# Kernel tuning notes

Measured on AMD Instinct MI355X. Metric: run time of the kernel, lower is better.

## Reference

```python
import jax, jax.numpy as jnp
import numpy as np

B, T, D_IN = 4096, 1024, 2
EMD, CELL, D_OUT = 128, 128, 5


def setup_inputs() -> dict:
    key = jax.random.key(0)
    ks = jax.random.split(key, 9)
    s = lambda k, shape, fan: jax.random.normal(k, shape, jnp.float32) / np.sqrt(fan)
    return {
        "inputs": jax.random.normal(ks[0], (B, T, D_IN), jnp.float32),
        "We": s(ks[1], (EMD, D_IN), D_IN),
        "be": s(ks[2], (EMD,), D_IN),
        "W_ih": s(ks[3], (4 * CELL, EMD), EMD),
        "W_hh": s(ks[4], (4 * CELL, CELL), CELL),
        "b_ih": s(ks[5], (4 * CELL,), CELL),
        "b_hh": s(ks[6], (4 * CELL,), CELL),
        "Wo": s(ks[7], (D_OUT, CELL), CELL),
        "bo": s(ks[8], (D_OUT,), CELL),
    }


def reference(inputs, We, be, W_ih, W_hh, b_ih, b_hh, Wo, bo):
    """VanillaLSTM forward: per-step embed MLP -> LSTMCell -> output MLP.
    inputs: [B, T, D_IN]; returns (outputs [B, T, D_OUT], h [B,CELL], c [B,CELL])."""
    Bsz = inputs.shape[0]
    cell = W_hh.shape[1]

    def step(hc, x_t):
        h, c = hc
        # input embedding MLP (Linear + ReLU, batch_norm=False)
        e = jax.nn.relu(x_t @ We.T + be)                      # [B, EMD]
        # torch.nn.LSTMCell gate math
        gates = e @ W_ih.T + b_ih + h @ W_hh.T + b_hh         # [B, 4*CELL]
        i, f, g, o = jnp.split(gates, 4, axis=-1)
        i, f, o = jax.nn.sigmoid(i), jax.nn.sigmoid(f), jax.nn.sigmoid(o)
        g = jnp.tanh(g)
        c_new = f * c + i * g
        h_new = o * jnp.tanh(c_new)
        # output embedding (Linear, no activation)
        y = h_new @ Wo.T + bo                                 # [B, D_OUT]
        return (h_new, c_new), y

    h0 = jnp.zeros((Bsz, cell), inputs.dtype)
    c0 = jnp.zeros((Bsz, cell), inputs.dtype)
    xs = jnp.swapaxes(inputs, 0, 1)                           # [T, B, D_IN]
    (h, c), ys = jax.lax.scan(step, (h0, c0), xs)
    outputs = jnp.swapaxes(ys, 0, 1)                          # [B, T, D_OUT]
    return outputs, h, c
```

## Files before the change

### kernel.cpp

```cpp
#include <hip/hip_runtime.h>
#include <hip/hip_bf16.h>


#define B_TOT 4096
#define T_LEN 1024
#define D_INP 2
#define EMD   128
#define CELL  128
#define D_OUT 5

#define ROWS  16
#define WAVES 8
#define BLOCK (WAVES * 64)
#define LDH   136

typedef short s8v  __attribute__((ext_vector_type(8)));
typedef short s4v  __attribute__((ext_vector_type(4)));
typedef float f32x4 __attribute__((ext_vector_type(4)));

#if __has_builtin(__builtin_amdgcn_exp2f)
#define EXP2F(x) __builtin_amdgcn_exp2f(x)
#else
#define EXP2F(x) exp2f(x)
#endif
#if __has_builtin(__builtin_amdgcn_rcpf)
#define RCPF(x) __builtin_amdgcn_rcpf(x)
#else
#define RCPF(x) (1.0f / (x))
#endif

__device__ __forceinline__ float bf2f(short s) {
    unsigned int u = ((unsigned int)(unsigned short)s) << 16;
    return __builtin_bit_cast(float, u);
}
__device__ __forceinline__ short f2bf(float f) {
    unsigned int u = __builtin_bit_cast(unsigned int, f);
    u += 0x7fffu + ((u >> 16) & 1u);
    return (short)(u >> 16);
}
__device__ __forceinline__ float sigm(float x) {
    return RCPF(1.0f + EXP2F(-1.44269504f * x));
}
__device__ __forceinline__ float tanh_fast(float x) {
    return 2.0f * RCPF(1.0f + EXP2F(-2.88539008f * x)) - 1.0f;
}
__device__ __forceinline__ s8v load8_f32_to_bf16(const float* p) {
    float4 a = *(const float4*)p;
    float4 b = *(const float4*)(p + 4);
    s8v r;
    r[0] = f2bf(a.x); r[1] = f2bf(a.y); r[2] = f2bf(a.z); r[3] = f2bf(a.w);
    r[4] = f2bf(b.x); r[5] = f2bf(b.y); r[6] = f2bf(b.z); r[7] = f2bf(b.w);
    return r;
}

__global__ __launch_bounds__(BLOCK, 1)
void lstm_persistent(const float* __restrict__ x,
                     const float* __restrict__ We,
                     const float* __restrict__ be,
                     const float* __restrict__ Wih,
                     const float* __restrict__ Whh,
                     const float* __restrict__ bih,
                     const float* __restrict__ bhh,
                     const float* __restrict__ Wo,
                     const float* __restrict__ bo,
                     float* __restrict__ out)
{
    __shared__ short h_lds[2][ROWS][LDH];
    __shared__ short e_lds[2][ROWS][LDH];

    const int tid  = threadIdx.x;
    const int lane = tid & 63;
    const int w    = tid >> 6;
    const int n16  = lane & 15;
    const int q    = lane >> 4;
    const int q8   = q * 8;
    const int b0   = blockIdx.x * ROWS;
    const int jcol = w * 16 + n16;

    float* out_y = out;
    float* out_h = out + (size_t)B_TOT * T_LEN * D_OUT;
    float* out_c = out_h + (size_t)B_TOT * CELL;

    s8v wih_f[4][4], whh_f[4][4];
    #pragma unroll
    for (int g = 0; g < 4; ++g) {
        const int row = g * CELL + jcol;
        #pragma unroll
        for (int kt = 0; kt < 4; ++kt) {
            wih_f[g][kt] = load8_f32_to_bf16(Wih + row * EMD  + kt * 32 + q8);
            whh_f[g][kt] = load8_f32_to_bf16(Whh + row * CELL + kt * 32 + q8);
        }
    }
    float bias_g[4];
    #pragma unroll
    for (int g = 0; g < 4; ++g)
        bias_g[g] = bih[g * CELL + jcol] + bhh[g * CELL + jcol];

    s8v wo_f[4];
    float bo_v = 0.0f;
    {
        s8v z = {0, 0, 0, 0, 0, 0, 0, 0};
        #pragma unroll
        for (int kt = 0; kt < 4; ++kt) wo_f[kt] = z;
        if (w == 0 && n16 < D_OUT) {
            #pragma unroll
            for (int kt = 0; kt < 4; ++kt)
                wo_f[kt] = load8_f32_to_bf16(Wo + n16 * CELL + kt * 32 + q8);
            bo_v = bo[n16];
        }
    }

    const int er  = tid >> 5;
    const int jj0 = (tid & 31) * 4;
    float weA[4], weB[4], bev[4];
    #pragma unroll
    for (int jl = 0; jl < 4; ++jl) {
        weA[jl] = We[(jj0 + jl) * 2 + 0];
        weB[jl] = We[(jj0 + jl) * 2 + 1];
        bev[jl] = be[jj0 + jl];
    }
    const float* xrow = x + (size_t)(b0 + er) * T_LEN * D_INP;

    {
        unsigned int* hz = (unsigned int*)&h_lds[0][0][0];
        for (int i = tid; i < ROWS * LDH / 2; i += BLOCK) hz[i] = 0u;

        float2 xd = *(const float2*)(xrow);
        s4v ev;
        #pragma unroll
        for (int jl = 0; jl < 4; ++jl)
            ev[jl] = f2bf(fmaxf(xd.x * weA[jl] + xd.y * weB[jl] + bev[jl], 0.0f));
        *(s4v*)&e_lds[0][er][jj0] = ev;
    }

    float c_r[4] = {0.0f, 0.0f, 0.0f, 0.0f};

    #pragma unroll 1
    for (int u = 0; u < T_LEN; ++u) {
        const int p = u & 1;
        __syncthreads();

        s8v ah[4], ae[4];
        #pragma unroll
        for (int kt = 0; kt < 4; ++kt) {
            ah[kt] = *(const s8v*)&h_lds[p][n16][kt * 32 + q8];
            ae[kt] = *(const s8v*)&e_lds[p][n16][kt * 32 + q8];
        }

        if (w == 0 && u > 0) {
            f32x4 ay = {bo_v, bo_v, bo_v, bo_v};
            #pragma unroll
            for (int kt = 0; kt < 4; ++kt)
                ay = __builtin_amdgcn_mfma_f32_16x16x32_bf16(ah[kt], wo_f[kt], ay, 0, 0, 0);
            if (n16 < D_OUT) {
                #pragma unroll
                for (int r = 0; r < 4; ++r)
                    out_y[((size_t)(b0 + q * 4 + r) * T_LEN + (u - 1)) * D_OUT + n16] = ay[r];
            }
        }

        f32x4 acc[4];
        #pragma unroll
        for (int g = 0; g < 4; ++g) {
            f32x4 a = {bias_g[g], bias_g[g], bias_g[g], bias_g[g]};
            #pragma unroll
            for (int kt = 0; kt < 4; ++kt) {
                a = __builtin_amdgcn_mfma_f32_16x16x32_bf16(ah[kt], whh_f[g][kt], a, 0, 0, 0);
                a = __builtin_amdgcn_mfma_f32_16x16x32_bf16(ae[kt], wih_f[g][kt], a, 0, 0, 0);
            }
            acc[g] = a;
        }

        #pragma unroll
        for (int r = 0; r < 4; ++r) {
            float iv = sigm(acc[0][r]);
            float fv = sigm(acc[1][r]);
            float gv = tanh_fast(acc[2][r]);
            float ov = sigm(acc[3][r]);
            c_r[r] = fv * c_r[r] + iv * gv;
            float hv = ov * tanh_fast(c_r[r]);
            h_lds[1 - p][q * 4 + r][jcol] = f2bf(hv);
        }

        {
            const int tn = (u + 1 < T_LEN) ? (u + 1) : (T_LEN - 1);
            float2 xd = *(const float2*)(xrow + tn * D_INP);
            s4v ev;
            #pragma unroll
            for (int jl = 0; jl < 4; ++jl)
                ev[jl] = f2bf(fmaxf(xd.x * weA[jl] + xd.y * weB[jl] + bev[jl], 0.0f));
            *(s4v*)&e_lds[1 - p][er][jj0] = ev;
        }
    }

    __syncthreads();

    if (w == 0) {
        s8v ah[4];
        #pragma unroll
        for (int kt = 0; kt < 4; ++kt)
            ah[kt] = *(const s8v*)&h_lds[0][n16][kt * 32 + q8];
        f32x4 ay = {bo_v, bo_v, bo_v, bo_v};
        #pragma unroll
        for (int kt = 0; kt < 4; ++kt)
            ay = __builtin_amdgcn_mfma_f32_16x16x32_bf16(ah[kt], wo_f[kt], ay, 0, 0, 0);
        if (n16 < D_OUT) {
            #pragma unroll
            for (int r = 0; r < 4; ++r)
                out_y[((size_t)(b0 + q * 4 + r) * T_LEN + (T_LEN - 1)) * D_OUT + n16] = ay[r];
        }
    }

    #pragma unroll
    for (int r = 0; r < 4; ++r)
        out_c[(size_t)(b0 + q * 4 + r) * CELL + jcol] = c_r[r];

    {
        const int m  = (tid * 4) >> 7;
        const int k0 = (tid * 4) & 127;
        s4v hv = *(const s4v*)&h_lds[0][m][k0];
        float4 hf;
        hf.x = bf2f(hv[0]); hf.y = bf2f(hv[1]);
        hf.z = bf2f(hv[2]); hf.w = bf2f(hv[3]);
        *(float4*)(out_h + (size_t)(b0 + m) * CELL + k0) = hf;
    }
}

extern "C" void kernel_launch(void* const* d_in, const int* in_sizes, int n_in,
                              void* d_out, int out_size, void* d_ws, size_t ws_size,
                              hipStream_t stream) {
    const float* x   = (const float*)d_in[0];
    const float* We  = (const float*)d_in[1];
    const float* be  = (const float*)d_in[2];
    const float* Wih = (const float*)d_in[3];
    const float* Whh = (const float*)d_in[4];
    const float* bih = (const float*)d_in[5];
    const float* bhh = (const float*)d_in[6];
    const float* Wo  = (const float*)d_in[7];
    const float* bo  = (const float*)d_in[8];
    float* out = (float*)d_out;

    dim3 grid(B_TOT / ROWS);
    dim3 block(BLOCK);
    hipLaunchKernelGGL(lstm_persistent, grid, block, 0, stream,
                       x, We, be, Wih, Whh, bih, bhh, Wo, bo, out);
}
```

Measured before the change: 1.398 ms.

## Transpose MFMA operands so each lane owns four channels and packs stores

Swaps the A/B operands of every MFMA so the accumulator holds four consecutive cell channels per lane for one batch row. This lets the h state be written to LDS as two packed 32-bit bf16 words instead of four scattered shorts, and lets the output y, c and final h be stored as contiguous vectors. It also replaces __syncthreads with a raw s_waitcnt lgkmcnt+s_barrier and hoists the next x load ahead of the MFMA work to hide global latency. The bf16 packing now rounds half-up instead of round-to-nearest-even, and the final h is written in fp32 rather than round-tripped through bf16.

Result: no change. 1.394 ms (-0.3%).

```diff
diff --git a/kernel.cpp b/kernel.cpp
--- a/kernel.cpp
+++ b/kernel.cpp
@@ -17,6 +17,8 @@
 typedef short s8v  __attribute__((ext_vector_type(8)));
 typedef short s4v  __attribute__((ext_vector_type(4)));
 typedef float f32x4 __attribute__((ext_vector_type(4)));
+
+#define BAR() asm volatile("s_waitcnt lgkmcnt(0)\n\ts_barrier" ::: "memory")
 
 #if __has_builtin(__builtin_amdgcn_exp2f)
 #define EXP2F(x) __builtin_amdgcn_exp2f(x)
@@ -37,6 +39,11 @@
     unsigned int u = __builtin_bit_cast(unsigned int, f);
     u += 0x7fffu + ((u >> 16) & 1u);
     return (short)(u >> 16);
+}
+__device__ __forceinline__ unsigned int pk_bf16(float a, float b) {
+    unsigned int ua = __builtin_bit_cast(unsigned int, a);
+    unsigned int ub = __builtin_bit_cast(unsigned int, b);
+    return ((ua + 0x8000u) >> 16) | ((ub + 0x8000u) & 0xffff0000u);
 }
 __device__ __forceinline__ float sigm(float x) {
     return RCPF(1.0f + EXP2F(-1.44269504f * x));
@@ -75,7 +82,7 @@
     const int q    = lane >> 4;
     const int q8   = q * 8;
     const int b0   = blockIdx.x * ROWS;
-    const int jcol = w * 16 + n16;
+    const int ch0  = w * 16 + q * 4;
 
     float* out_y = out;
     float* out_h = out + (size_t)B_TOT * T_LEN * D_OUT;
@@ -84,20 +91,23 @@
     s8v wih_f[4][4], whh_f[4][4];
     #pragma unroll
     for (int g = 0; g < 4; ++g) {
-        const int row = g * CELL + jcol;
+        const int row = g * CELL + w * 16 + n16;
         #pragma unroll
         for (int kt = 0; kt < 4; ++kt) {
             wih_f[g][kt] = load8_f32_to_bf16(Wih + row * EMD  + kt * 32 + q8);
             whh_f[g][kt] = load8_f32_to_bf16(Whh + row * CELL + kt * 32 + q8);
         }
     }
-    float bias_g[4];
+    float4 bias4[4];
     #pragma unroll
-    for (int g = 0; g < 4; ++g)
-        bias_g[g] = bih[g * CELL + jcol] + bhh[g * CELL + jcol];
+    for (int g = 0; g < 4; ++g) {
+        float4 bi = *(const float4*)(bih + g * CELL + ch0);
+        float4 bh = *(const float4*)(bhh + g * CELL + ch0);
+        bias4[g] = make_float4(bi.x + bh.x, bi.y + bh.y, bi.z + bh.z, bi.w + bh.w);
+    }
 
     s8v wo_f[4];
-    float bo_v = 0.0f;
+    float bo_r[4];
     {
         s8v z = {0, 0, 0, 0, 0, 0, 0, 0};
         #pragma unroll
@@ -106,7 +116,11 @@
             #pragma unroll
             for (int kt = 0; kt < 4; ++kt)
                 wo_f[kt] = load8_f32_to_bf16(Wo + n16 * CELL + kt * 32 + q8);
-            bo_v = bo[n16];
+        }
+        #pragma unroll
+        for (int r = 0; r < 4; ++r) {
+            const int oc = q * 4 + r;
+            bo_r[r] = (w == 0 && oc < D_OUT) ? bo[oc] : 0.0f;
         }
     }
 
@@ -126,11 +140,13 @@
         for (int i = tid; i < ROWS * LDH / 2; i += BLOCK) hz[i] = 0u;
 
         float2 xd = *(const float2*)(xrow);
-        s4v ev;
-        #pragma unroll
-        for (int jl = 0; jl < 4; ++jl)
-            ev[jl] = f2bf(fmaxf(xd.x * weA[jl] + xd.y * weB[jl] + bev[jl], 0.0f));
-        *(s4v*)&e_lds[0][er][jj0] = ev;
+        float e0 = fmaxf(xd.x * weA[0] + xd.y * weB[0] + bev[0], 0.0f);
+        float e1 = fmaxf(xd.x * weA[1] + xd.y * weB[1] + bev[1], 0.0f);
+        float e2 = fmaxf(xd.x * weA[2] + xd.y * weB[2] + bev[2], 0.0f);
+        float e3 = fmaxf(xd.x * weA[3] + xd.y * weB[3] + bev[3], 0.0f);
+        unsigned int u01 = pk_bf16(e0, e1), u23 = pk_bf16(e2, e3);
+        *(unsigned int*)&e_lds[0][er][jj0]     = u01;
+        *(unsigned int*)&e_lds[0][er][jj0 + 2] = u23;
     }
 
     float c_r[4] = {0.0f, 0.0f, 0.0f, 0.0f};
@@ -138,7 +154,10 @@
     #pragma unroll 1
     for (int u = 0; u < T_LEN; ++u) {
         const int p = u & 1;
-        __syncthreads();
+        BAR();
+
+        const int tn = (u + 1 < T_LEN) ? (u + 1) : (T_LEN - 1);
+        float2 xd = *(const float2*)(xrow + tn * D_INP);
 
         s8v ah[4], ae[4];
         #pragma unroll
@@ -148,29 +167,31 @@
         }
 
         if (w == 0 && u > 0) {
-            f32x4 ay = {bo_v, bo_v, bo_v, bo_v};
+            f32x4 ay = {bo_r[0], bo_r[1], bo_r[2], bo_r[3]};
             #pragma unroll
             for (int kt = 0; kt < 4; ++kt)
-                ay = __builtin_amdgcn_mfma_f32_16x16x32_bf16(ah[kt], wo_f[kt], ay, 0, 0, 0);
-            if (n16 < D_OUT) {
-                #pragma unroll
-                for (int r = 0; r < 4; ++r)
-                    out_y[((size_t)(b0 + q * 4 + r) * T_LEN + (u - 1)) * D_OUT + n16] = ay[r];
+                ay = __builtin_amdgcn_mfma_f32_16x16x32_bf16(wo_f[kt], ah[kt], ay, 0, 0, 0);
+            float* yp = out_y + ((size_t)(b0 + n16) * T_LEN + (u - 1)) * D_OUT;
+            if (q == 0) {
+                yp[0] = ay[0]; yp[1] = ay[1]; yp[2] = ay[2]; yp[3] = ay[3];
+            } else if (q == 1) {
+                yp[4] = ay[0];
             }
         }
 
         f32x4 acc[4];
         #pragma unroll
         for (int g = 0; g < 4; ++g) {
-            f32x4 a = {bias_g[g], bias_g[g], bias_g[g], bias_g[g]};
+            f32x4 a = {bias4[g].x, bias4[g].y, bias4[g].z, bias4[g].w};
             #pragma unroll
             for (int kt = 0; kt < 4; ++kt) {
-                a = __builtin_amdgcn_mfma_f32_16x16x32_bf16(ah[kt], whh_f[g][kt], a, 0, 0, 0);
-                a = __builtin_amdgcn_mfma_f32_16x16x32_bf16(ae[kt], wih_f[g][kt], a, 0, 0, 0);
+                a = __builtin_amdgcn_mfma_f32_16x16x32_bf16(whh_f[g][kt], ah[kt], a, 0, 0, 0);
+                a = __builtin_amdgcn_mfma_f32_16x16x32_bf16(wih_f[g][kt], ae[kt], a, 0, 0, 0);
             }
             acc[g] = a;
         }
 
+        float hv[4];
         #pragma unroll
         for (int r = 0; r < 4; ++r) {
             float iv = sigm(acc[0][r]);
@@ -178,52 +199,51 @@
             float gv = tanh_fast(acc[2][r]);
             float ov = sigm(acc[3][r]);
             c_r[r] = fv * c_r[r] + iv * gv;
-            float hv = ov * tanh_fast(c_r[r]);
-            h_lds[1 - p][q * 4 + r][jcol] = f2bf(hv);
-        }
-
+            hv[r] = ov * tanh_fast(c_r[r]);
+        }
         {
-            const int tn = (u + 1 < T_LEN) ? (u + 1) : (T_LEN - 1);
-            float2 xd = *(const float2*)(xrow + tn * D_INP);
-            s4v ev;
-            #pragma unroll
-            for (int jl = 0; jl < 4; ++jl)
-                ev[jl] = f2bf(fmaxf(xd.x * weA[jl] + xd.y * weB[jl] + bev[jl], 0.0f));
-            *(s4v*)&e_lds[1 - p][er][jj0] = ev;
-        }
-    }
-
-    __syncthreads();
+            unsigned int u01 = pk_bf16(hv[0], hv[1]);
+            unsigned int u23 = pk_bf16(hv[2], hv[3]);
+            unsigned int* hp = (unsigned int*)&h_lds[1 - p][n16][ch0];
+            hp[0] = u01; hp[1] = u23;
+        }
+        if (u == T_LEN - 1) {
+            *(float4*)(out_h + (size_t)(b0 + n16) * CELL + ch0) =
+                make_float4(hv[0], hv[1], hv[2], hv[3]);
+        }
+
+        {
+            float e0 = fmaxf(xd.x * weA[0] + xd.y * weB[0] + bev[0], 0.0f);
+            float e1 = fmaxf(xd.x * weA[1] + xd.y * weB[1] + bev[1], 0.0f);
+            float e2 = fmaxf(xd.x * weA[2] + xd.y * weB[2] + bev[2], 0.0f);
+            float e3 = fmaxf(xd.x * weA[3] + xd.y * weB[3] + bev[3], 0.0f);
+            unsigned int u01 = pk_bf16(e0, e1), u23 = pk_bf16(e2, e3);
+            unsigned int* ep = (unsigned int*)&e_lds[1 - p][er][jj0];
+            ep[0] = u01; ep[1] = u23;
+        }
+    }
+
+    BAR();
 
     if (w == 0) {
         s8v ah[4];
         #pragma unroll
         for (int kt = 0; kt < 4; ++kt)
             ah[kt] = *(const s8v*)&h_lds[0][n16][kt * 32 + q8];
-        f32x4 ay = {bo_v, bo_v, bo_v, bo_v};
+        f32x4 ay = {bo_r[0], bo_r[1], bo_r[2], bo_r[3]};
         #pragma unroll
         for (int kt = 0; kt < 4; ++kt)
-            ay = __builtin_amdgcn_mfma_f32_16x16x32_bf16(ah[kt], wo_f[kt], ay, 0, 0, 0);
-        if (n16 < D_OUT) {
-            #pragma unroll
-            for (int r = 0; r < 4; ++r)
-                out_y[((size_t)(b0 + q * 4 + r) * T_LEN + (T_LEN - 1)) * D_OUT + n16] = ay[r];
-        }
-    }
-
-    #pragma unroll
-    for (int r = 0; r < 4; ++r)
-        out_c[(size_t)(b0 + q * 4 + r) * CELL + jcol] = c_r[r];
-
-    {
-        const int m  = (tid * 4) >> 7;
-        const int k0 = (tid * 4) & 127;
-        s4v hv = *(const s4v*)&h_lds[0][m][k0];
-        float4 hf;
-        hf.x = bf2f(hv[0]); hf.y = bf2f(hv[1]);
-        hf.z = bf2f(hv[2]); hf.w = bf2f(hv[3]);
-        *(float4*)(out_h + (size_t)(b0 + m) * CELL + k0) = hf;
-    }
+            ay = __builtin_amdgcn_mfma_f32_16x16x32_bf16(wo_f[kt], ah[kt], ay, 0, 0, 0);
+        float* yp = out_y + ((size_t)(b0 + n16) * T_LEN + (T_LEN - 1)) * D_OUT;
+        if (q == 0) {
+            yp[0] = ay[0]; yp[1] = ay[1]; yp[2] = ay[2]; yp[3] = ay[3];
+        } else if (q == 1) {
+            yp[4] = ay[0];
+        }
+    }
+
+    *(float4*)(out_c + (size_t)(b0 + n16) * CELL + ch0) =
+        make_float4(c_r[0], c_r[1], c_r[2], c_r[3]);
 }
 
 extern "C" void kernel_launch(void* const* d_in, const int* in_sizes, int n_in,
```
